# Optimization experiments

Hardware: AMD Instinct MI355X
Metric: run time of the kernel (lower is better)

Reference implementation:

```python
import jax, jax.numpy as jnp
import numpy as np

E = 16          # n_routed_experts
D = 2048        # embedding_dim
H = 1408        # moe_inter_dim
HS = 2 * 1408   # shared expert hidden (n_shared_experts * moe_inter_dim)
TOP_K = 6
ROUTE_SCALE = 1.0


def setup_inputs() -> dict:
    key = jax.random.key(0)
    ks = jax.random.split(key, 16)
    s = 0.02
    return {
        "x": jax.random.normal(ks[0], (4, 1024, D), dtype=jnp.float32),
        "gate_w": jax.random.normal(ks[1], (E, D), dtype=jnp.float32) * s,
        "gate_b": jax.random.normal(ks[2], (E,), dtype=jnp.float32) * s,
        "w1": jax.random.normal(ks[3], (E, H, D), dtype=jnp.float32) * s,
        "b1": jax.random.normal(ks[4], (E, H), dtype=jnp.float32) * s,
        "w2": jax.random.normal(ks[5], (E, D, H), dtype=jnp.float32) * s,
        "b2": jax.random.normal(ks[6], (E, D), dtype=jnp.float32) * s,
        "w3": jax.random.normal(ks[7], (E, H, D), dtype=jnp.float32) * s,
        "b3": jax.random.normal(ks[8], (E, H), dtype=jnp.float32) * s,
        "ws1": jax.random.normal(ks[9], (HS, D), dtype=jnp.float32) * s,
        "bs1": jax.random.normal(ks[10], (HS,), dtype=jnp.float32) * s,
        "ws2": jax.random.normal(ks[11], (D, HS), dtype=jnp.float32) * s,
        "bs2": jax.random.normal(ks[12], (D,), dtype=jnp.float32) * s,
        "ws3": jax.random.normal(ks[13], (HS, D), dtype=jnp.float32) * s,
        "bs3": jax.random.normal(ks[14], (HS,), dtype=jnp.float32) * s,
    }


def reference(x, gate_w, gate_b, w1, b1, w2, b2, w3, b3, ws1, bs1, ws2, bs2, ws3, bs3):
    shape = x.shape
    xf = x.reshape(-1, shape[-1])                       # [T, D]
    # --- Gate ---
    scores = xf @ gate_w.T                              # [T, E]
    probs = jax.nn.softmax(scores.astype(jnp.float32), axis=-1)
    biased = probs + gate_b                             # bias added after softmax
    _, idx = jax.lax.top_k(biased, TOP_K)               # [T, K]
    weights = jnp.take_along_axis(probs, idx, axis=1) * ROUTE_SCALE
    weights = weights.astype(x.dtype)                   # [T, K]
    # Combine weights as dense [T, E] (sum of top-k routing weights per expert)
    onehot = jax.nn.one_hot(idx, E, dtype=weights.dtype)  # [T, K, E]
    cw = jnp.einsum('tk,tke->te', weights, onehot)        # [T, E]
    # --- Routed experts: scan over experts, accumulate weighted SwiGLU outputs ---
    def expert_step(y, params):
        W1, B1, W2, B2, W3, B3, c = params              # c: [T]
        h = jax.nn.silu(xf @ W1.T + B1) * (xf @ W3.T + B3)  # [T, H]
        out = h @ W2.T + B2                             # [T, D]
        return y + c[:, None] * out, None
    y0 = jnp.zeros_like(xf)
    y, _ = jax.lax.scan(expert_step, y0, (w1, b1, w2, b2, w3, b3, cw.T))
    # --- Shared experts (dense SwiGLU MLP) ---
    z = (jax.nn.silu(xf @ ws1.T + bs1) * (xf @ ws3.T + bs3)) @ ws2.T + bs2
    return (y + z).reshape(shape)
```

## Files before the change

kernel.cpp:

```cpp
#include <hip/hip_runtime.h>

#define NE 16
#define DD 2048
#define HH 1408
#define HSH 2816
#define TOPK 6
#define TT 4096

typedef __bf16 bf16x8 __attribute__((ext_vector_type(8)));
typedef __bf16 bf16x4 __attribute__((ext_vector_type(4)));
typedef float f32x4 __attribute__((ext_vector_type(4)));

typedef const __attribute__((address_space(1))) void gvoid_t;
typedef __attribute__((address_space(3))) void lvoid_t;

__device__ __forceinline__ void gll16(const void* g, void* l) {
  __builtin_amdgcn_global_load_lds((gvoid_t*)g, (lvoid_t*)l, 16, 0, 0);
}

__global__ void k_cvt(const float* __restrict__ s, __bf16* __restrict__ d, long n4) {
  long i = (long)blockIdx.x * blockDim.x + threadIdx.x;
  long stride = (long)gridDim.x * blockDim.x;
  for (; i < n4; i += stride) {
    float4 v = ((const float4*)s)[i];
    bf16x4 o = { (__bf16)v.x, (__bf16)v.y, (__bf16)v.z, (__bf16)v.w };
    ((bf16x4*)d)[i] = o;
  }
}

__global__ __launch_bounds__(256) void k_gate(
    const float* __restrict__ x, const float* __restrict__ gw,
    const float* __restrict__ gb, float* __restrict__ cw,
    int* __restrict__ counts, int* __restrict__ lists,
    int* __restrict__ tok_e, int* __restrict__ tok_pos) {
  int t = blockIdx.x;
  int lane = threadIdx.x & 63, wave = threadIdx.x >> 6;
  __shared__ float sc[NE];
  const float* xt = x + (size_t)t * DD;
  for (int ei = 0; ei < 4; ++ei) {
    int e = wave * 4 + ei;
    const float* ge = gw + (size_t)e * DD;
    float s = 0.f;
    for (int j = 0; j < DD / 64; ++j) s += xt[lane + 64 * j] * ge[lane + 64 * j];
    for (int o = 32; o; o >>= 1) s += __shfl_xor(s, o);
    if (lane == 0) sc[e] = s;
  }
  __syncthreads();
  if (threadIdx.x == 0) {
    float p[NE], b[NE];
    float m = -1e30f;
    for (int e = 0; e < NE; ++e) m = fmaxf(m, sc[e]);
    float sum = 0.f;
    for (int e = 0; e < NE; ++e) { p[e] = expf(sc[e] - m); sum += p[e]; }
    float inv = 1.f / sum;
    for (int e = 0; e < NE; ++e) { p[e] *= inv; b[e] = p[e] + gb[e]; }
    float out[NE];
    bool used[NE];
    for (int e = 0; e < NE; ++e) { out[e] = 0.f; used[e] = false; }
    for (int k = 0; k < TOPK; ++k) {
      int best = -1; float bv = -1e30f;
      for (int e = 0; e < NE; ++e)
        if (!used[e] && b[e] > bv) { bv = b[e]; best = e; }
      used[best] = true;
      out[best] = p[best];
      int pos = atomicAdd(&counts[best], 1);
      lists[best * TT + pos] = t;
      tok_e[t * TOPK + k] = best;
      tok_pos[t * TOPK + k] = pos;
    }
    for (int e = 0; e < NE; ++e) cw[(size_t)t * NE + e] = out[e];
  }
}

__global__ void k_offsets(const int* __restrict__ counts, int* __restrict__ offs) {
  if (threadIdx.x == 0) {
    int a = 0;
    for (int e = 0; e < NE; ++e) { offs[e] = a; a += counts[e]; }
    offs[NE] = a;
  }
}

template <bool GATHER>
__global__ __launch_bounds__(256, 4) void k_gemm1(
    const __bf16* __restrict__ xb,
    const __bf16* __restrict__ W1, const float* __restrict__ B1,
    const __bf16* __restrict__ W3, const float* __restrict__ B3,
    __bf16* __restrict__ Hout, int Hdim,
    const int* __restrict__ counts, const int* __restrict__ offs,
    const int* __restrict__ lists) {
  int e = blockIdx.z;
  int count = GATHER ? counts[e] : TT;
  int m0 = blockIdx.y * 128;
  if (m0 >= count) return;
  int n0 = blockIdx.x * 64;
  const __bf16* W1e = W1 + (size_t)e * Hdim * DD;
  const __bf16* W3e = W3 + (size_t)e * Hdim * DD;
  const float* B1e = B1 + (size_t)e * Hdim;
  const float* B3e = B3 + (size_t)e * Hdim;
  int hbase = GATHER ? offs[e] : 0;
  const int* liste = GATHER ? lists + (size_t)e * TT : nullptr;

  __shared__ __bf16 At[128 * 64];
  __shared__ __bf16 B1t[64 * 64];
  __shared__ __bf16 B3t[64 * 64];
  __shared__ int rowtok[128];

  int tid = threadIdx.x, lane = tid & 63, wave = tid >> 6;
  if (tid < 128) {
    int s = m0 + tid;
    rowtok[tid] = GATHER ? liste[s < count ? s : 0] : (m0 + tid);
  }
  __syncthreads();

  int wm = wave >> 1, wn = wave & 1;
  f32x4 acc1[4][2] = {};
  f32x4 acc3[4][2] = {};
  int lr8 = lane >> 3;
  int lc8 = (lane & 7) * 8;
  int fr = lane & 15;
  int fk = (lane >> 4) * 8;

  for (int k0 = 0; k0 < DD; k0 += 64) {
    #pragma unroll
    for (int c = 0; c < 4; ++c) {
      int br = c * 32 + wave * 8;
      int tok = rowtok[br + lr8];
      gll16(xb + (size_t)tok * DD + k0 + lc8, &At[br * 64]);
    }
    #pragma unroll
    for (int c = 0; c < 2; ++c) {
      int br = c * 32 + wave * 8;
      gll16(W1e + (size_t)(n0 + br + lr8) * DD + k0 + lc8, &B1t[br * 64]);
      gll16(W3e + (size_t)(n0 + br + lr8) * DD + k0 + lc8, &B3t[br * 64]);
    }
    __syncthreads();
    #pragma unroll
    for (int kk = 0; kk < 2; ++kk) {
      bf16x8 af[4], b1f[2], b3f[2];
      #pragma unroll
      for (int m = 0; m < 4; ++m)
        af[m] = *(const bf16x8*)&At[(wm * 64 + m * 16 + fr) * 64 + kk * 32 + fk];
      #pragma unroll
      for (int n = 0; n < 2; ++n) {
        b1f[n] = *(const bf16x8*)&B1t[(wn * 32 + n * 16 + fr) * 64 + kk * 32 + fk];
        b3f[n] = *(const bf16x8*)&B3t[(wn * 32 + n * 16 + fr) * 64 + kk * 32 + fk];
      }
      #pragma unroll
      for (int m = 0; m < 4; ++m)
        #pragma unroll
        for (int n = 0; n < 2; ++n) {
          acc1[m][n] = __builtin_amdgcn_mfma_f32_16x16x32_bf16(af[m], b1f[n], acc1[m][n], 0, 0, 0);
          acc3[m][n] = __builtin_amdgcn_mfma_f32_16x16x32_bf16(af[m], b3f[n], acc3[m][n], 0, 0, 0);
        }
    }
    __syncthreads();
  }
  #pragma unroll
  for (int m = 0; m < 4; ++m)
    #pragma unroll
    for (int n = 0; n < 2; ++n)
      #pragma unroll
      for (int j = 0; j < 4; ++j) {
        int rl = wm * 64 + m * 16 + (lane >> 4) * 4 + j;
        int s = m0 + rl;
        if (s < count) {
          int col = n0 + wn * 32 + n * 16 + fr;
          float h1 = acc1[m][n][j] + B1e[col];
          float h3 = acc3[m][n][j] + B3e[col];
          float v = h1 / (1.f + expf(-h1)) * h3;
          Hout[(size_t)(hbase + s) * Hdim + col] = (__bf16)v;
        }
      }
}

template <bool GATHER>
__global__ __launch_bounds__(256, 4) void k_gemm2(
    const __bf16* __restrict__ Hsrc, int Kd,
    const __bf16* __restrict__ W2, const float* __restrict__ B2,
    float* __restrict__ out, __bf16* __restrict__ Ybuf,
    const int* __restrict__ counts, const int* __restrict__ offs) {
  int e = blockIdx.z;
  int count = GATHER ? counts[e] : TT;
  int m0 = blockIdx.y * 128;
  if (m0 >= count) return;
  int n0 = blockIdx.x * 128;
  int hbase = GATHER ? offs[e] : 0;
  const __bf16* Ae = Hsrc + (size_t)hbase * Kd;
  const __bf16* W2e = W2 + (size_t)e * DD * Kd;
  const float* B2e = B2 + (size_t)(GATHER ? e * DD : 0);

  __shared__ __bf16 At[128 * 64];
  __shared__ __bf16 Bt[128 * 64];

  int tid = threadIdx.x, lane = tid & 63, wave = tid >> 6;
  int wm = wave >> 1, wn = wave & 1;
  f32x4 acc[4][4] = {};
  int lr8 = lane >> 3;
  int lc8 = (lane & 7) * 8;
  int fr = lane & 15;
  int fk = (lane >> 4) * 8;

  for (int k0 = 0; k0 < Kd; k0 += 64) {
    #pragma unroll
    for (int c = 0; c < 4; ++c) {
      int br = c * 32 + wave * 8;
      int sr = m0 + br + lr8;
      if (sr >= count) sr = count - 1;
      gll16(Ae + (size_t)sr * Kd + k0 + lc8, &At[br * 64]);
      gll16(W2e + (size_t)(n0 + br + lr8) * Kd + k0 + lc8, &Bt[br * 64]);
    }
    __syncthreads();
    #pragma unroll
    for (int kk = 0; kk < 2; ++kk) {
      bf16x8 af[4], bf[4];
      #pragma unroll
      for (int m = 0; m < 4; ++m)
        af[m] = *(const bf16x8*)&At[(wm * 64 + m * 16 + fr) * 64 + kk * 32 + fk];
      #pragma unroll
      for (int n = 0; n < 4; ++n)
        bf[n] = *(const bf16x8*)&Bt[(wn * 64 + n * 16 + fr) * 64 + kk * 32 + fk];
      #pragma unroll
      for (int m = 0; m < 4; ++m)
        #pragma unroll
        for (int n = 0; n < 4; ++n)
          acc[m][n] = __builtin_amdgcn_mfma_f32_16x16x32_bf16(af[m], bf[n], acc[m][n], 0, 0, 0);
    }
    __syncthreads();
  }
  #pragma unroll
  for (int m = 0; m < 4; ++m)
    #pragma unroll
    for (int n = 0; n < 4; ++n)
      #pragma unroll
      for (int j = 0; j < 4; ++j) {
        int rl = wm * 64 + m * 16 + (lane >> 4) * 4 + j;
        int s = m0 + rl;
        if (s < count) {
          int d = n0 + wn * 64 + n * 16 + fr;
          float v = acc[m][n][j] + B2e[d];
          if (GATHER)
            Ybuf[(size_t)(hbase + s) * DD + d] = (__bf16)v;
          else
            out[(size_t)s * DD + d] = v;
        }
      }
}

__global__ __launch_bounds__(256) void k_combine(
    const __bf16* __restrict__ Ybuf, const float* __restrict__ cw,
    const int* __restrict__ offs, const int* __restrict__ tok_e,
    const int* __restrict__ tok_pos, float* __restrict__ out) {
  int t = blockIdx.x;
  int tid = threadIdx.x;
  __shared__ int rws[TOPK];
  __shared__ float wsh[TOPK];
  if (tid < TOPK) {
    int e = tok_e[t * TOPK + tid];
    rws[tid] = offs[e] + tok_pos[t * TOPK + tid];
    wsh[tid] = cw[(size_t)t * NE + e];
  }
  __syncthreads();
  int d0 = tid * 8;
  float a[8];
  float4 o0 = *(const float4*)&out[(size_t)t * DD + d0];
  float4 o1 = *(const float4*)&out[(size_t)t * DD + d0 + 4];
  a[0] = o0.x; a[1] = o0.y; a[2] = o0.z; a[3] = o0.w;
  a[4] = o1.x; a[5] = o1.y; a[6] = o1.z; a[7] = o1.w;
  #pragma unroll
  for (int k = 0; k < TOPK; ++k) {
    bf16x8 v = *(const bf16x8*)&Ybuf[(size_t)rws[k] * DD + d0];
    float w = wsh[k];
    #pragma unroll
    for (int j = 0; j < 8; ++j) a[j] += w * (float)v[j];
  }
  float4 r0 = { a[0], a[1], a[2], a[3] };
  float4 r1 = { a[4], a[5], a[6], a[7] };
  *(float4*)&out[(size_t)t * DD + d0] = r0;
  *(float4*)&out[(size_t)t * DD + d0 + 4] = r1;
}

extern "C" void kernel_launch(void* const* d_in, const int* in_sizes, int n_in,
                              void* d_out, int out_size, void* d_ws, size_t ws_size,
                              hipStream_t stream) {
  const float* x      = (const float*)d_in[0];
  const float* gate_w = (const float*)d_in[1];
  const float* gate_b = (const float*)d_in[2];
  const float* w1     = (const float*)d_in[3];
  const float* b1     = (const float*)d_in[4];
  const float* w2     = (const float*)d_in[5];
  const float* b2     = (const float*)d_in[6];
  const float* w3     = (const float*)d_in[7];
  const float* b3     = (const float*)d_in[8];
  const float* ws1    = (const float*)d_in[9];
  const float* bs1    = (const float*)d_in[10];
  const float* ws2    = (const float*)d_in[11];
  const float* bs2    = (const float*)d_in[12];
  const float* ws3    = (const float*)d_in[13];
  const float* bs3    = (const float*)d_in[14];
  float* outp = (float*)d_out;

  char* ws = (char*)d_ws;
  size_t off = 0;
  auto take = [&](size_t bytes) { char* p = ws + off; off += (bytes + 255) & ~(size_t)255; return p; };
  __bf16* xb   = (__bf16*)take((size_t)TT * DD * 2);
  __bf16* w1b  = (__bf16*)take((size_t)NE * HH * DD * 2);
  __bf16* w3b  = (__bf16*)take((size_t)NE * HH * DD * 2);
  __bf16* w2b  = (__bf16*)take((size_t)NE * DD * HH * 2);
  __bf16* ws1b = (__bf16*)take((size_t)HSH * DD * 2);
  __bf16* ws3b = (__bf16*)take((size_t)HSH * DD * 2);
  __bf16* ws2b = (__bf16*)take((size_t)DD * HSH * 2);
  __bf16* Hbuf = (__bf16*)take((size_t)TT * TOPK * HH * 2);
  __bf16* Sbuf = (__bf16*)take((size_t)TT * HSH * 2);
  float*  cw   = (float*)take((size_t)TT * NE * 4);
  int*    lists  = (int*)take((size_t)NE * TT * 4);
  int*    tok_e  = (int*)take((size_t)TT * TOPK * 4);
  int*    tok_pos= (int*)take((size_t)TT * TOPK * 4);
  int*    counts = (int*)take(64);
  int*    offs   = (int*)take(128);
  __bf16* Ybuf = w1b;

  hipMemsetAsync(counts, 0, NE * sizeof(int), stream);

  k_cvt<<<2048, 256, 0, stream>>>(x, xb, (long)TT * DD / 4);
  k_cvt<<<2048, 256, 0, stream>>>(w1, w1b, (long)NE * HH * DD / 4);
  k_cvt<<<2048, 256, 0, stream>>>(w3, w3b, (long)NE * HH * DD / 4);
  k_cvt<<<2048, 256, 0, stream>>>(w2, w2b, (long)NE * DD * HH / 4);
  k_cvt<<<2048, 256, 0, stream>>>(ws1, ws1b, (long)HSH * DD / 4);
  k_cvt<<<2048, 256, 0, stream>>>(ws3, ws3b, (long)HSH * DD / 4);
  k_cvt<<<2048, 256, 0, stream>>>(ws2, ws2b, (long)DD * HSH / 4);

  k_gate<<<TT, 256, 0, stream>>>(x, gate_w, gate_b, cw, counts, lists, tok_e, tok_pos);
  k_offsets<<<1, 64, 0, stream>>>(counts, offs);

  k_gemm1<true><<<dim3(HH / 64, TT / 128, NE), 256, 0, stream>>>(
      xb, w1b, b1, w3b, b3, Hbuf, HH, counts, offs, lists);
  k_gemm1<false><<<dim3(HSH / 64, TT / 128, 1), 256, 0, stream>>>(
      xb, ws1b, bs1, ws3b, bs3, Sbuf, HSH, nullptr, nullptr, nullptr);
  k_gemm2<true><<<dim3(DD / 128, TT / 128, NE), 256, 0, stream>>>(
      Hbuf, HH, w2b, b2, nullptr, Ybuf, counts, offs);
  k_gemm2<false><<<dim3(DD / 128, TT / 128, 1), 256, 0, stream>>>(
      Sbuf, HSH, ws2b, bs2, outp, nullptr, nullptr, nullptr);
  k_combine<<<TT, 256, 0, stream>>>(Ybuf, cw, offs, tok_e, tok_pos, outp);
}
```

Baseline: 1.374 ms.

## Rewrite expert GEMMs with 256-wide tiles, double-buffered LDS, swizzle and interleaved prefetch

Both GEMM kernels move to 512-thread blocks with 256x128 or 256x256 tiles. They use two LDS buffers with a swizzled layout to avoid bank conflicts and interleave global-to-LDS prefetch of the next K tiles with MFMA phases under explicit barriers, vmcnt waits and setprio. The seven weight conversion launches are merged into one segmented kernel. Larger tiles raise reuse and cut launch overhead, but reduce grid occupancy for small per-expert counts and rely on fragile manual wait counts.

```diff
diff --git a/kernel.cpp b/kernel.cpp
--- a/kernel.cpp
+++ b/kernel.cpp
@@ -18,13 +18,31 @@
   __builtin_amdgcn_global_load_lds((gvoid_t*)g, (lvoid_t*)l, 16, 0, 0);
 }
 
-__global__ void k_cvt(const float* __restrict__ s, __bf16* __restrict__ d, long n4) {
+__device__ __forceinline__ f32x4 MF(bf16x8 a, bf16x8 b, f32x4 c) {
+  return __builtin_amdgcn_mfma_f32_16x16x32_bf16(a, b, c, 0, 0, 0);
+}
+
+#define BAR() do { asm volatile("" ::: "memory"); __builtin_amdgcn_s_barrier(); asm volatile("" ::: "memory"); } while (0)
+#define WAITV8() asm volatile("s_waitcnt vmcnt(8)" ::: "memory")
+#define WAITV0() asm volatile("s_waitcnt vmcnt(0)" ::: "memory")
+#define WAITL0() asm volatile("s_waitcnt lgkmcnt(0)" ::: "memory")
+
+struct Cvt7 {
+  const float* src[7];
+  __bf16* dst[7];
+  long off[8];
+};
+__global__ __launch_bounds__(256) void k_cvt_all(Cvt7 c) {
   long i = (long)blockIdx.x * blockDim.x + threadIdx.x;
   long stride = (long)gridDim.x * blockDim.x;
-  for (; i < n4; i += stride) {
-    float4 v = ((const float4*)s)[i];
+  long total = c.off[7];
+  for (; i < total; i += stride) {
+    int seg = 0;
+    while (i >= c.off[seg + 1]) ++seg;
+    long j = i - c.off[seg];
+    float4 v = ((const float4*)c.src[seg])[j];
     bf16x4 o = { (__bf16)v.x, (__bf16)v.y, (__bf16)v.z, (__bf16)v.w };
-    ((bf16x4*)d)[i] = o;
+    ((bf16x4*)c.dst[seg])[j] = o;
   }
 }
 
@@ -81,7 +99,7 @@
 }
 
 template <bool GATHER>
-__global__ __launch_bounds__(256, 4) void k_gemm1(
+__global__ __launch_bounds__(512, 1) void k_g1(
     const __bf16* __restrict__ xb,
     const __bf16* __restrict__ W1, const float* __restrict__ B1,
     const __bf16* __restrict__ W3, const float* __restrict__ B3,
@@ -90,9 +108,9 @@
     const int* __restrict__ lists) {
   int e = blockIdx.z;
   int count = GATHER ? counts[e] : TT;
-  int m0 = blockIdx.y * 128;
+  int m0 = blockIdx.y * 256;
   if (m0 >= count) return;
-  int n0 = blockIdx.x * 64;
+  int n0 = blockIdx.x * 128;
   const __bf16* W1e = W1 + (size_t)e * Hdim * DD;
   const __bf16* W3e = W3 + (size_t)e * Hdim * DD;
   const float* B1e = B1 + (size_t)e * Hdim;
@@ -100,73 +118,134 @@
   int hbase = GATHER ? offs[e] : 0;
   const int* liste = GATHER ? lists + (size_t)e * TT : nullptr;
 
-  __shared__ __bf16 At[128 * 64];
-  __shared__ __bf16 B1t[64 * 64];
-  __shared__ __bf16 B3t[64 * 64];
-  __shared__ int rowtok[128];
-
-  int tid = threadIdx.x, lane = tid & 63, wave = tid >> 6;
-  if (tid < 128) {
+  __shared__ __bf16 At[2][256 * 64];
+  __shared__ __bf16 B1t[2][128 * 64];
+  __shared__ __bf16 B3t[2][128 * 64];
+  __shared__ int rowtok[256];
+
+  int tid = threadIdx.x, lane = tid & 63, w = tid >> 6;
+  int wm = w >> 2, wn = w & 3;
+  if (tid < 256) {
     int s = m0 + tid;
-    rowtok[tid] = GATHER ? liste[s < count ? s : 0] : (m0 + tid);
+    rowtok[tid] = GATHER ? liste[s < count ? s : count - 1] : (m0 + tid);
   }
   __syncthreads();
 
-  int wm = wave >> 1, wn = wave & 1;
-  f32x4 acc1[4][2] = {};
-  f32x4 acc3[4][2] = {};
-  int lr8 = lane >> 3;
-  int lc8 = (lane & 7) * 8;
+  int l8 = lane >> 3;
+  int p8 = lane & 7;
+  int sw8 = p8 ^ l8;
   int fr = lane & 15;
-  int fk = (lane >> 4) * 8;
-
-  for (int k0 = 0; k0 < DD; k0 += 64) {
+  int g4 = lane >> 4;
+  int h7 = lane & 7;
+
+  auto stageA = [&](int buf, int kt) {
+    int k0 = kt * 64;
     #pragma unroll
     for (int c = 0; c < 4; ++c) {
-      int br = c * 32 + wave * 8;
-      int tok = rowtok[br + lr8];
-      gll16(xb + (size_t)tok * DD + k0 + lc8, &At[br * 64]);
-    }
+      int rb = c * 64 + w * 8;
+      int tok = rowtok[rb + l8];
+      gll16(xb + (size_t)tok * DD + k0 + sw8 * 8, &At[buf][rb * 64]);
+    }
+  };
+  auto stageB = [&](int buf, int kt) {
+    int k0 = kt * 64;
     #pragma unroll
     for (int c = 0; c < 2; ++c) {
-      int br = c * 32 + wave * 8;
-      gll16(W1e + (size_t)(n0 + br + lr8) * DD + k0 + lc8, &B1t[br * 64]);
-      gll16(W3e + (size_t)(n0 + br + lr8) * DD + k0 + lc8, &B3t[br * 64]);
-    }
-    __syncthreads();
-    #pragma unroll
-    for (int kk = 0; kk < 2; ++kk) {
-      bf16x8 af[4], b1f[2], b3f[2];
-      #pragma unroll
-      for (int m = 0; m < 4; ++m)
-        af[m] = *(const bf16x8*)&At[(wm * 64 + m * 16 + fr) * 64 + kk * 32 + fk];
-      #pragma unroll
-      for (int n = 0; n < 2; ++n) {
-        b1f[n] = *(const bf16x8*)&B1t[(wn * 32 + n * 16 + fr) * 64 + kk * 32 + fk];
-        b3f[n] = *(const bf16x8*)&B3t[(wn * 32 + n * 16 + fr) * 64 + kk * 32 + fk];
+      int rb = c * 64 + w * 8;
+      int r = rb + l8;
+      gll16(W1e + (size_t)(n0 + r) * DD + k0 + sw8 * 8, &B1t[buf][rb * 64]);
+      gll16(W3e + (size_t)(n0 + r) * DD + k0 + sw8 * 8, &B3t[buf][rb * 64]);
+    }
+  };
+
+  f32x4 acc1[8][2] = {};
+  f32x4 acc3[8][2] = {};
+
+  stageB(0, 0); stageA(0, 0);
+  stageB(1, 1); stageA(1, 1);
+  WAITV8(); BAR();
+
+  const int nk = DD / 64;
+  for (int k = 0; k < nk; ++k) {
+    int cur = k & 1;
+    bf16x8 a0[8], a1[8], b1f[2][2], b3f[2][2];
+    #pragma unroll
+    for (int nf = 0; nf < 2; ++nf)
+      #pragma unroll
+      for (int kk = 0; kk < 2; ++kk) {
+        int rr = wn * 32 + nf * 16 + fr;
+        int p = (kk * 4 + g4) ^ h7;
+        b1f[nf][kk] = *(const bf16x8*)&B1t[cur][rr * 64 + p * 8];
+        b3f[nf][kk] = *(const bf16x8*)&B3t[cur][rr * 64 + p * 8];
       }
-      #pragma unroll
-      for (int m = 0; m < 4; ++m)
-        #pragma unroll
-        for (int n = 0; n < 2; ++n) {
-          acc1[m][n] = __builtin_amdgcn_mfma_f32_16x16x32_bf16(af[m], b1f[n], acc1[m][n], 0, 0, 0);
-          acc3[m][n] = __builtin_amdgcn_mfma_f32_16x16x32_bf16(af[m], b3f[n], acc3[m][n], 0, 0, 0);
-        }
-    }
-    __syncthreads();
-  }
+    #pragma unroll
+    for (int mf = 0; mf < 8; ++mf) {
+      int rr = wm * 128 + mf * 16 + fr;
+      int p = g4 ^ h7;
+      a0[mf] = *(const bf16x8*)&At[cur][rr * 64 + p * 8];
+    }
+    BAR();
+    __builtin_amdgcn_s_setprio(1);
+    #pragma unroll
+    for (int mf = 0; mf < 8; ++mf)
+      #pragma unroll
+      for (int nf = 0; nf < 2; ++nf)
+        acc1[mf][nf] = MF(a0[mf], b1f[nf][0], acc1[mf][nf]);
+    __builtin_amdgcn_s_setprio(0);
+    WAITL0();
+    BAR();
+    #pragma unroll
+    for (int mf = 0; mf < 8; ++mf) {
+      int rr = wm * 128 + mf * 16 + fr;
+      int p = (4 + g4) ^ h7;
+      a1[mf] = *(const bf16x8*)&At[cur][rr * 64 + p * 8];
+    }
+    if (k + 2 < nk) stageB(cur, k + 2);
+    BAR();
+    __builtin_amdgcn_s_setprio(1);
+    #pragma unroll
+    for (int mf = 0; mf < 8; ++mf)
+      #pragma unroll
+      for (int nf = 0; nf < 2; ++nf)
+        acc3[mf][nf] = MF(a0[mf], b3f[nf][0], acc3[mf][nf]);
+    __builtin_amdgcn_s_setprio(0);
+    WAITL0();
+    BAR();
+    if (k + 2 < nk) stageA(cur, k + 2);
+    BAR();
+    __builtin_amdgcn_s_setprio(1);
+    #pragma unroll
+    for (int mf = 0; mf < 8; ++mf)
+      #pragma unroll
+      for (int nf = 0; nf < 2; ++nf)
+        acc1[mf][nf] = MF(a1[mf], b1f[nf][1], acc1[mf][nf]);
+    __builtin_amdgcn_s_setprio(0);
+    BAR();
+    if (k + 2 < nk) { WAITV8(); }
+    else if (k + 1 < nk) { WAITV0(); }
+    BAR();
+    __builtin_amdgcn_s_setprio(1);
+    #pragma unroll
+    for (int mf = 0; mf < 8; ++mf)
+      #pragma unroll
+      for (int nf = 0; nf < 2; ++nf)
+        acc3[mf][nf] = MF(a1[mf], b3f[nf][1], acc3[mf][nf]);
+    __builtin_amdgcn_s_setprio(0);
+    BAR();
+  }
+
   #pragma unroll
-  for (int m = 0; m < 4; ++m)
-    #pragma unroll
-    for (int n = 0; n < 2; ++n)
+  for (int mf = 0; mf < 8; ++mf)
+    #pragma unroll
+    for (int nf = 0; nf < 2; ++nf)
       #pragma unroll
       for (int j = 0; j < 4; ++j) {
-        int rl = wm * 64 + m * 16 + (lane >> 4) * 4 + j;
+        int rl = wm * 128 + mf * 16 + (lane >> 4) * 4 + j;
         int s = m0 + rl;
         if (s < count) {
-          int col = n0 + wn * 32 + n * 16 + fr;
-          float h1 = acc1[m][n][j] + B1e[col];
-          float h3 = acc3[m][n][j] + B3e[col];
+          int col = n0 + wn * 32 + nf * 16 + fr;
+          float h1 = acc1[mf][nf][j] + B1e[col];
+          float h3 = acc3[mf][nf][j] + B3e[col];
           float v = h1 / (1.f + expf(-h1)) * h3;
           Hout[(size_t)(hbase + s) * Hdim + col] = (__bf16)v;
         }
@@ -174,70 +253,139 @@
 }
 
 template <bool GATHER>
-__global__ __launch_bounds__(256, 4) void k_gemm2(
+__global__ __launch_bounds__(512, 1) void k_g2(
     const __bf16* __restrict__ Hsrc, int Kd,
     const __bf16* __restrict__ W2, const float* __restrict__ B2,
     float* __restrict__ out, __bf16* __restrict__ Ybuf,
     const int* __restrict__ counts, const int* __restrict__ offs) {
   int e = blockIdx.z;
   int count = GATHER ? counts[e] : TT;
-  int m0 = blockIdx.y * 128;
+  int m0 = blockIdx.y * 256;
   if (m0 >= count) return;
-  int n0 = blockIdx.x * 128;
+  int n0 = blockIdx.x * 256;
   int hbase = GATHER ? offs[e] : 0;
   const __bf16* Ae = Hsrc + (size_t)hbase * Kd;
   const __bf16* W2e = W2 + (size_t)e * DD * Kd;
   const float* B2e = B2 + (size_t)(GATHER ? e * DD : 0);
 
-  __shared__ __bf16 At[128 * 64];
-  __shared__ __bf16 Bt[128 * 64];
-
-  int tid = threadIdx.x, lane = tid & 63, wave = tid >> 6;
-  int wm = wave >> 1, wn = wave & 1;
-  f32x4 acc[4][4] = {};
-  int lr8 = lane >> 3;
-  int lc8 = (lane & 7) * 8;
+  __shared__ __bf16 At[2][256 * 64];
+  __shared__ __bf16 Bt[2][256 * 64];
+
+  int tid = threadIdx.x, lane = tid & 63, w = tid >> 6;
+  int wm = w >> 2, wn = w & 3;
+
+  int l8 = lane >> 3;
+  int p8 = lane & 7;
+  int sw8 = p8 ^ l8;
   int fr = lane & 15;
-  int fk = (lane >> 4) * 8;
-
-  for (int k0 = 0; k0 < Kd; k0 += 64) {
+  int g4 = lane >> 4;
+  int h7 = lane & 7;
+
+  auto stageA = [&](int buf, int kt) {
+    int k0 = kt * 64;
     #pragma unroll
     for (int c = 0; c < 4; ++c) {
-      int br = c * 32 + wave * 8;
-      int sr = m0 + br + lr8;
+      int rb = c * 64 + w * 8;
+      int sr = m0 + rb + l8;
       if (sr >= count) sr = count - 1;
-      gll16(Ae + (size_t)sr * Kd + k0 + lc8, &At[br * 64]);
-      gll16(W2e + (size_t)(n0 + br + lr8) * Kd + k0 + lc8, &Bt[br * 64]);
-    }
-    __syncthreads();
-    #pragma unroll
-    for (int kk = 0; kk < 2; ++kk) {
-      bf16x8 af[4], bf[4];
-      #pragma unroll
-      for (int m = 0; m < 4; ++m)
-        af[m] = *(const bf16x8*)&At[(wm * 64 + m * 16 + fr) * 64 + kk * 32 + fk];
-      #pragma unroll
-      for (int n = 0; n < 4; ++n)
-        bf[n] = *(const bf16x8*)&Bt[(wn * 64 + n * 16 + fr) * 64 + kk * 32 + fk];
-      #pragma unroll
-      for (int m = 0; m < 4; ++m)
-        #pragma unroll
-        for (int n = 0; n < 4; ++n)
-          acc[m][n] = __builtin_amdgcn_mfma_f32_16x16x32_bf16(af[m], bf[n], acc[m][n], 0, 0, 0);
-    }
-    __syncthreads();
-  }
+      gll16(Ae + (size_t)sr * Kd + k0 + sw8 * 8, &At[buf][rb * 64]);
+    }
+  };
+  auto stageB = [&](int buf, int kt) {
+    int k0 = kt * 64;
+    #pragma unroll
+    for (int c = 0; c < 4; ++c) {
+      int rb = c * 64 + w * 8;
+      int r = rb + l8;
+      gll16(W2e + (size_t)(n0 + r) * Kd + k0 + sw8 * 8, &Bt[buf][rb * 64]);
+    }
+  };
+
+  f32x4 acc[8][4] = {};
+
+  stageB(0, 0); stageA(0, 0);
+  stageB(1, 1); stageA(1, 1);
+  WAITV8(); BAR();
+
+  const int nk = Kd / 64;
+  for (int k = 0; k < nk; ++k) {
+    int cur = k & 1;
+    bf16x8 a0[8], a1[8], bf[4][2];
+    #pragma unroll
+    for (int nf = 0; nf < 4; ++nf)
+      #pragma unroll
+      for (int kk = 0; kk < 2; ++kk) {
+        int rr = wn * 64 + nf * 16 + fr;
+        int p = (kk * 4 + g4) ^ h7;
+        bf[nf][kk] = *(const bf16x8*)&Bt[cur][rr * 64 + p * 8];
+      }
+    #pragma unroll
+    for (int mf = 0; mf < 8; ++mf) {
+      int rr = wm * 128 + mf * 16 + fr;
+      int p = g4 ^ h7;
+      a0[mf] = *(const bf16x8*)&At[cur][rr * 64 + p * 8];
+    }
+    BAR();
+    __builtin_amdgcn_s_setprio(1);
+    #pragma unroll
+    for (int mf = 0; mf < 8; ++mf)
+      #pragma unroll
+      for (int nf = 0; nf < 2; ++nf)
+        acc[mf][nf] = MF(a0[mf], bf[nf][0], acc[mf][nf]);
+    __builtin_amdgcn_s_setprio(0);
+    WAITL0();
+    BAR();
+    #pragma unroll
+    for (int mf = 0; mf < 8; ++mf) {
+      int rr = wm * 128 + mf * 16 + fr;
+      int p = (4 + g4) ^ h7;
+      a1[mf] = *(const bf16x8*)&At[cur][rr * 64 + p * 8];
+    }
+    if (k + 2 < nk) stageB(cur, k + 2);
+    BAR();
+    __builtin_amdgcn_s_setprio(1);
+    #pragma unroll
+    for (int mf = 0; mf < 8; ++mf)
+      #pragma unroll
+      for (int nf = 2; nf < 4; ++nf)
+        acc[mf][nf] = MF(a0[mf], bf[nf][0], acc[mf][nf]);
+    __builtin_amdgcn_s_setprio(0);
+    WAITL0();
+    BAR();
+    if (k + 2 < nk) stageA(cur, k + 2);
+    BAR();
+    __builtin_amdgcn_s_setprio(1);
+    #pragma unroll
+    for (int mf = 0; mf < 8; ++mf)
+      #pragma unroll
+      for (int nf = 0; nf < 2; ++nf)
+        acc[mf][nf] = MF(a1[mf], bf[nf][1], acc[mf][nf]);
+    __builtin_amdgcn_s_setprio(0);
+    BAR();
+    if (k + 2 < nk) { WAITV8(); }
+    else if (k + 1 < nk) { WAITV0(); }
+    BAR();
+    __builtin_amdgcn_s_setprio(1);
+    #pragma unroll
+    for (int mf = 0; mf < 8; ++mf)
+      #pragma unroll
+      for (int nf = 2; nf < 4; ++nf)
+        acc[mf][nf] = MF(a1[mf], bf[nf][1], acc[mf][nf]);
+    __builtin_amdgcn_s_setprio(0);
+    BAR();
+  }
+
   #pragma unroll
-  for (int m = 0; m < 4; ++m)
-    #pragma unroll
-    for (int n = 0; n < 4; ++n)
+  for (int mf = 0; mf < 8; ++mf)
+    #pragma unroll
+    for (int nf = 0; nf < 4; ++nf)
       #pragma unroll
       for (int j = 0; j < 4; ++j) {
-        int rl = wm * 64 + m * 16 + (lane >> 4) * 4 + j;
+        int rl = wm * 128 + mf * 16 + (lane >> 4) * 4 + j;
         int s = m0 + rl;
         if (s < count) {
-          int d = n0 + wn * 64 + n * 16 + fr;
-          float v = acc[m][n][j] + B2e[d];
+          int d = n0 + wn * 64 + nf * 16 + fr;
+          float v = acc[mf][nf][j] + B2e[d];
           if (GATHER)
             Ybuf[(size_t)(hbase + s) * DD + d] = (__bf16)v;
           else
@@ -321,24 +469,26 @@
 
   hipMemsetAsync(counts, 0, NE * sizeof(int), stream);
 
-  k_cvt<<<2048, 256, 0, stream>>>(x, xb, (long)TT * DD / 4);
-  k_cvt<<<2048, 256, 0, stream>>>(w1, w1b, (long)NE * HH * DD / 4);
-  k_cvt<<<2048, 256, 0, stream>>>(w3, w3b, (long)NE * HH * DD / 4);
-  k_cvt<<<2048, 256, 0, stream>>>(w2, w2b, (long)NE * DD * HH / 4);
-  k_cvt<<<2048, 256, 0, stream>>>(ws1, ws1b, (long)HSH * DD / 4);
-  k_cvt<<<2048, 256, 0, stream>>>(ws3, ws3b, (long)HSH * DD / 4);
-  k_cvt<<<2048, 256, 0, stream>>>(ws2, ws2b, (long)DD * HSH / 4);
+  Cvt7 c;
+  const float* srcs[7] = { x, w1, w3, w2, ws1, ws3, ws2 };
+  __bf16* dsts[7] = { xb, w1b, w3b, w2b, ws1b, ws3b, ws2b };
+  long sz4[7] = { (long)TT * DD / 4, (long)NE * HH * DD / 4, (long)NE * HH * DD / 4,
+                  (long)NE * DD * HH / 4, (long)HSH * DD / 4, (long)HSH * DD / 4,
+                  (long)DD * HSH / 4 };
+  c.off[0] = 0;
+  for (int i = 0; i < 7; ++i) { c.src[i] = srcs[i]; c.dst[i] = dsts[i]; c.off[i + 1] = c.off[i] + sz4[i]; }
+  k_cvt_all<<<4096, 256, 0, stream>>>(c);
 
   k_gate<<<TT, 256, 0, stream>>>(x, gate_w, gate_b, cw, counts, lists, tok_e, tok_pos);
   k_offsets<<<1, 64, 0, stream>>>(counts, offs);
 
-  k_gemm1<true><<<dim3(HH / 64, TT / 128, NE), 256, 0, stream>>>(
+  k_g1<true><<<dim3(HH / 128, TT / 256, NE), 512, 0, stream>>>(
       xb, w1b, b1, w3b, b3, Hbuf, HH, counts, offs, lists);
-  k_gemm1<false><<<dim3(HSH / 64, TT / 128, 1), 256, 0, stream>>>(
+  k_g1<false><<<dim3(HSH / 128, TT / 256, 1), 512, 0, stream>>>(
       xb, ws1b, bs1, ws3b, bs3, Sbuf, HSH, nullptr, nullptr, nullptr);
-  k_gemm2<true><<<dim3(DD / 128, TT / 128, NE), 256, 0, stream>>>(
+  k_g2<true><<<dim3(DD / 256, TT / 256, NE), 512, 0, stream>>>(
       Hbuf, HH, w2b, b2, nullptr, Ybuf, counts, offs);
-  k_gemm2<false><<<dim3(DD / 128, TT / 128, 1), 256, 0, stream>>>(
+  k_g2<false><<<dim3(DD / 256, TT / 256, 1), 512, 0, stream>>>(
       Sbuf, HSH, ws2b, bs2, outp, nullptr, nullptr, nullptr);
   k_combine<<<TT, 256, 0, stream>>>(Ybuf, cw, offs, tok_e, tok_pos, outp);
 }
```

After: 1.443 ms. +5.0%, slower.

## Merge conversion launches and fuse routed and shared expert GEMMs into single grids

Applied to the files above, without the earlier changes.

Folds the seven fp32-to-bf16 conversion launches into one kernel that walks a segment table. Merges the routed-expert and shared-expert GEMM1 launches into one grid with an extra z slice, and does the same for GEMM2. This removes launch gaps and lets the shared and routed tiles fill the GPU together. GEMM1 also keeps token indices in registers instead of a shared-memory table with a barrier, and raises the launch-bounds occupancy hint to 5. Costs: the per-element segment search in the conversion kernel, and many early-exit blocks in the padded GEMM1 grid.

```diff
diff --git a/kernel.cpp b/kernel.cpp
--- a/kernel.cpp
+++ b/kernel.cpp
@@ -18,13 +18,22 @@
   __builtin_amdgcn_global_load_lds((gvoid_t*)g, (lvoid_t*)l, 16, 0, 0);
 }
 
-__global__ void k_cvt(const float* __restrict__ s, __bf16* __restrict__ d, long n4) {
+struct Cvt7 {
+  const float* src[7];
+  __bf16* dst[7];
+  long off[8];
+};
+__global__ __launch_bounds__(256) void k_cvt_all(Cvt7 c) {
   long i = (long)blockIdx.x * blockDim.x + threadIdx.x;
   long stride = (long)gridDim.x * blockDim.x;
-  for (; i < n4; i += stride) {
-    float4 v = ((const float4*)s)[i];
+  long total = c.off[7];
+  for (; i < total; i += stride) {
+    int seg = 0;
+    while (i >= c.off[seg + 1]) ++seg;
+    long j = i - c.off[seg];
+    float4 v = ((const float4*)c.src[seg])[j];
     bf16x4 o = { (__bf16)v.x, (__bf16)v.y, (__bf16)v.z, (__bf16)v.w };
-    ((bf16x4*)d)[i] = o;
+    ((bf16x4*)c.dst[seg])[j] = o;
   }
 }
 
@@ -80,43 +89,51 @@
   }
 }
 
-template <bool GATHER>
-__global__ __launch_bounds__(256, 4) void k_gemm1(
+__global__ __launch_bounds__(256, 5) void k_g1m(
     const __bf16* __restrict__ xb,
-    const __bf16* __restrict__ W1, const float* __restrict__ B1,
-    const __bf16* __restrict__ W3, const float* __restrict__ B3,
-    __bf16* __restrict__ Hout, int Hdim,
+    const __bf16* __restrict__ W1r, const float* __restrict__ B1r,
+    const __bf16* __restrict__ W3r, const float* __restrict__ B3r,
+    const __bf16* __restrict__ W1s, const float* __restrict__ B1s,
+    const __bf16* __restrict__ W3s, const float* __restrict__ B3s,
+    __bf16* __restrict__ Hr, __bf16* __restrict__ Hs,
     const int* __restrict__ counts, const int* __restrict__ offs,
     const int* __restrict__ lists) {
-  int e = blockIdx.z;
-  int count = GATHER ? counts[e] : TT;
+  int z = blockIdx.z;
+  bool sh = (z == NE);
+  int gxmax = sh ? (HSH / 64) : (HH / 64);
+  if ((int)blockIdx.x >= gxmax) return;
+  int count = sh ? TT : counts[z];
   int m0 = blockIdx.y * 128;
   if (m0 >= count) return;
   int n0 = blockIdx.x * 64;
-  const __bf16* W1e = W1 + (size_t)e * Hdim * DD;
-  const __bf16* W3e = W3 + (size_t)e * Hdim * DD;
-  const float* B1e = B1 + (size_t)e * Hdim;
-  const float* B3e = B3 + (size_t)e * Hdim;
-  int hbase = GATHER ? offs[e] : 0;
-  const int* liste = GATHER ? lists + (size_t)e * TT : nullptr;
+  int Hdim = sh ? HSH : HH;
+  const __bf16* W1e = sh ? W1s : W1r + (size_t)z * HH * DD;
+  const __bf16* W3e = sh ? W3s : W3r + (size_t)z * HH * DD;
+  const float* B1e = sh ? B1s : B1r + (size_t)z * HH;
+  const float* B3e = sh ? B3s : B3r + (size_t)z * HH;
+  __bf16* Hout = sh ? Hs : Hr;
+  int hbase = sh ? 0 : offs[z];
+  const int* liste = lists + (size_t)z * TT;
 
   __shared__ __bf16 At[128 * 64];
   __shared__ __bf16 B1t[64 * 64];
   __shared__ __bf16 B3t[64 * 64];
-  __shared__ int rowtok[128];
 
   int tid = threadIdx.x, lane = tid & 63, wave = tid >> 6;
-  if (tid < 128) {
-    int s = m0 + tid;
-    rowtok[tid] = GATHER ? liste[s < count ? s : 0] : (m0 + tid);
-  }
-  __syncthreads();
+  int lr8 = lane >> 3;
+  int lc8 = (lane & 7) * 8;
+
+  int tokr[4];
+  #pragma unroll
+  for (int c = 0; c < 4; ++c) {
+    int row = m0 + c * 32 + wave * 8 + lr8;
+    if (row >= count) row = count - 1;
+    tokr[c] = sh ? row : liste[row];
+  }
 
   int wm = wave >> 1, wn = wave & 1;
   f32x4 acc1[4][2] = {};
   f32x4 acc3[4][2] = {};
-  int lr8 = lane >> 3;
-  int lc8 = (lane & 7) * 8;
   int fr = lane & 15;
   int fk = (lane >> 4) * 8;
 
@@ -124,8 +141,7 @@
     #pragma unroll
     for (int c = 0; c < 4; ++c) {
       int br = c * 32 + wave * 8;
-      int tok = rowtok[br + lr8];
-      gll16(xb + (size_t)tok * DD + k0 + lc8, &At[br * 64]);
+      gll16(xb + (size_t)tokr[c] * DD + k0 + lc8, &At[br * 64]);
     }
     #pragma unroll
     for (int c = 0; c < 2; ++c) {
@@ -173,21 +189,23 @@
       }
 }
 
-template <bool GATHER>
-__global__ __launch_bounds__(256, 4) void k_gemm2(
-    const __bf16* __restrict__ Hsrc, int Kd,
-    const __bf16* __restrict__ W2, const float* __restrict__ B2,
+__global__ __launch_bounds__(256, 4) void k_g2m(
+    const __bf16* __restrict__ Hr, const __bf16* __restrict__ Hs,
+    const __bf16* __restrict__ W2r, const float* __restrict__ B2r,
+    const __bf16* __restrict__ W2s, const float* __restrict__ B2s,
     float* __restrict__ out, __bf16* __restrict__ Ybuf,
     const int* __restrict__ counts, const int* __restrict__ offs) {
-  int e = blockIdx.z;
-  int count = GATHER ? counts[e] : TT;
+  int z = blockIdx.z;
+  bool sh = (z == NE);
+  int Kd = sh ? HSH : HH;
+  int count = sh ? TT : counts[z];
   int m0 = blockIdx.y * 128;
   if (m0 >= count) return;
   int n0 = blockIdx.x * 128;
-  int hbase = GATHER ? offs[e] : 0;
-  const __bf16* Ae = Hsrc + (size_t)hbase * Kd;
-  const __bf16* W2e = W2 + (size_t)e * DD * Kd;
-  const float* B2e = B2 + (size_t)(GATHER ? e * DD : 0);
+  int hbase = sh ? 0 : offs[z];
+  const __bf16* Ae = sh ? Hs : Hr + (size_t)hbase * HH;
+  const __bf16* W2e = sh ? W2s : W2r + (size_t)z * DD * HH;
+  const float* B2e = sh ? B2s : B2r + (size_t)z * DD;
 
   __shared__ __bf16 At[128 * 64];
   __shared__ __bf16 Bt[128 * 64];
@@ -238,7 +256,7 @@
         if (s < count) {
           int d = n0 + wn * 64 + n * 16 + fr;
           float v = acc[m][n][j] + B2e[d];
-          if (GATHER)
+          if (!sh)
             Ybuf[(size_t)(hbase + s) * DD + d] = (__bf16)v;
           else
             out[(size_t)s * DD + d] = v;
@@ -321,24 +339,23 @@
 
   hipMemsetAsync(counts, 0, NE * sizeof(int), stream);
 
-  k_cvt<<<2048, 256, 0, stream>>>(x, xb, (long)TT * DD / 4);
-  k_cvt<<<2048, 256, 0, stream>>>(w1, w1b, (long)NE * HH * DD / 4);
-  k_cvt<<<2048, 256, 0, stream>>>(w3, w3b, (long)NE * HH * DD / 4);
-  k_cvt<<<2048, 256, 0, stream>>>(w2, w2b, (long)NE * DD * HH / 4);
-  k_cvt<<<2048, 256, 0, stream>>>(ws1, ws1b, (long)HSH * DD / 4);
-  k_cvt<<<2048, 256, 0, stream>>>(ws3, ws3b, (long)HSH * DD / 4);
-  k_cvt<<<2048, 256, 0, stream>>>(ws2, ws2b, (long)DD * HSH / 4);
+  Cvt7 c;
+  const float* srcs[7] = { x, w1, w3, w2, ws1, ws3, ws2 };
+  __bf16* dsts[7] = { xb, w1b, w3b, w2b, ws1b, ws3b, ws2b };
+  long sz4[7] = { (long)TT * DD / 4, (long)NE * HH * DD / 4, (long)NE * HH * DD / 4,
+                  (long)NE * DD * HH / 4, (long)HSH * DD / 4, (long)HSH * DD / 4,
+                  (long)DD * HSH / 4 };
+  c.off[0] = 0;
+  for (int i = 0; i < 7; ++i) { c.src[i] = srcs[i]; c.dst[i] = dsts[i]; c.off[i + 1] = c.off[i] + sz4[i]; }
+  k_cvt_all<<<4096, 256, 0, stream>>>(c);
 
   k_gate<<<TT, 256, 0, stream>>>(x, gate_w, gate_b, cw, counts, lists, tok_e, tok_pos);
   k_offsets<<<1, 64, 0, stream>>>(counts, offs);
 
-  k_gemm1<true><<<dim3(HH / 64, TT / 128, NE), 256, 0, stream>>>(
-      xb, w1b, b1, w3b, b3, Hbuf, HH, counts, offs, lists);
-  k_gemm1<false><<<dim3(HSH / 64, TT / 128, 1), 256, 0, stream>>>(
-      xb, ws1b, bs1, ws3b, bs3, Sbuf, HSH, nullptr, nullptr, nullptr);
-  k_gemm2<true><<<dim3(DD / 128, TT / 128, NE), 256, 0, stream>>>(
-      Hbuf, HH, w2b, b2, nullptr, Ybuf, counts, offs);
-  k_gemm2<false><<<dim3(DD / 128, TT / 128, 1), 256, 0, stream>>>(
-      Sbuf, HSH, ws2b, bs2, outp, nullptr, nullptr, nullptr);
+  k_g1m<<<dim3(HSH / 64, TT / 128, NE + 1), 256, 0, stream>>>(
+      xb, w1b, b1, w3b, b3, ws1b, bs1, ws3b, bs3,
+      Hbuf, Sbuf, counts, offs, lists);
+  k_g2m<<<dim3(DD / 128, TT / 128, NE + 1), 256, 0, stream>>>(
+      Hbuf, Sbuf, w2b, b2, ws2b, bs2, outp, Ybuf, counts, offs);
   k_combine<<<TT, 256, 0, stream>>>(Ybuf, cw, offs, tok_e, tok_pos, outp);
 }
```

After: 2.366 ms. 72.2% more time.
